# Kernel tuning notes

Measured on AMD Instinct MI355X. Metric: run time of the kernel, lower is better.

The kernel has to match this reference:

```python
import jax, jax.numpy as jnp
import numpy as np

N, E, G = 100000, 1600000, 1024
BN_EPS = 1e-5
NEG_SLOPE = 0.2


def setup_inputs() -> dict:
    key = jax.random.key(0)
    ks = jax.random.split(key, 8)
    x = jax.random.normal(ks[0], (N, 128), dtype=jnp.float32)
    edge_index = jax.random.randint(ks[1], (2, E), 0, N, dtype=jnp.int64)
    batch = jnp.sort(jax.random.randint(ks[2], (N,), 0, G, dtype=jnp.int64))
    Wl = jax.random.normal(ks[3], (3, 128, 128), dtype=jnp.float32) * 0.08
    bl = jnp.zeros((3, 128), dtype=jnp.float32)
    Wr = jax.random.normal(ks[4], (3, 128, 128), dtype=jnp.float32) * 0.08
    bn_gamma = jnp.ones((3, 128), dtype=jnp.float32)
    bn_beta = jnp.zeros((3, 128), dtype=jnp.float32)
    bn2_gamma = jnp.ones((128,), dtype=jnp.float32)
    bn2_beta = jnp.zeros((128,), dtype=jnp.float32)
    fc_W = jax.random.normal(ks[5], (128, 64), dtype=jnp.float32) * 0.08
    fc_b = jnp.zeros((64,), dtype=jnp.float32)
    return {"x": x, "edge_index": edge_index, "batch": batch, "Wl": Wl, "bl": bl,
            "Wr": Wr, "bn_gamma": bn_gamma, "bn_beta": bn_beta,
            "bn2_gamma": bn2_gamma, "bn2_beta": bn2_beta, "fc_W": fc_W, "fc_b": fc_b}


def _batch_norm(h, gamma, beta):
    # training-mode BatchNorm1d: batch statistics, biased variance
    mu = jnp.mean(h, axis=0)
    var = jnp.mean((h - mu) ** 2, axis=0)
    return gamma * (h - mu) * jax.lax.rsqrt(var + BN_EPS) + beta


def reference(x, edge_index, batch, Wl, bl, Wr, bn_gamma, bn_beta,
              bn2_gamma, bn2_beta, fc_W, fc_b):
    src, dst = edge_index[0], edge_index[1]
    # in-degree of each destination node (for mean aggregation)
    deg = jax.ops.segment_sum(jnp.ones((E,), dtype=x.dtype), dst, num_segments=N)
    inv_deg = jnp.where(deg > 0, 1.0 / jnp.maximum(deg, 1.0), 0.0)[:, None]  # [N,1]
    h = x
    for i in range(3):
        # SAGEConv: out = lin_l(mean_{j in N(i)} h_j) + lin_r(h_i)
        agg = jax.ops.segment_sum(h[src], dst, num_segments=N) * inv_deg  # [N,H]
        h = agg @ Wl[i] + bl[i] + h @ Wr[i]
        h = jax.nn.leaky_relu(_batch_norm(h, bn_gamma[i], bn_beta[i]), NEG_SLOPE)
        # dropout omitted (eval-mode / deterministic reference)
    pooled = jax.ops.segment_sum(h, batch, num_segments=G)  # [G,H] global_add_pool
    out = _batch_norm(pooled, bn2_gamma, bn2_beta) @ fc_W + fc_b  # [G,latent]
    return out
```

## Files before the change

kernel.cpp:

```cpp
#include <hip/hip_runtime.h>

#define HD 128
#define NCOPY 32
#define BSH 8
#define BSZ 256
#define EPB 4096

typedef __attribute__((ext_vector_type(8))) short short8;
typedef __attribute__((ext_vector_type(4))) float f32x4;

union ABu { unsigned long long u[2]; short8 s8; };

__device__ inline float bf2f(ushort u) {
    union { unsigned int i; float f; } x; x.i = ((unsigned int)u) << 16; return x.f;
}
__device__ inline float bflo(unsigned int u) {
    union { unsigned int i; float f; } x; x.i = u << 16; return x.f;
}
__device__ inline float bfhi(unsigned int u) {
    union { unsigned int i; float f; } x; x.i = u & 0xffff0000u; return x.f;
}
__device__ inline ushort f2bf(float f) {
    union { float f; unsigned int i; } x; x.f = f;
    unsigned int r = x.i + 0x7FFF + ((x.i >> 16) & 1);
    return (ushort)(r >> 16);
}

__global__ __launch_bounds__(256) void k_prepcount(
        const float* __restrict__ x, ushort* __restrict__ xb, int total4,
        const float* __restrict__ Wl, const float* __restrict__ Wr,
        ushort* __restrict__ WT, int wtTotal,
        const int* __restrict__ dst, int* __restrict__ bucketCount, int E, int NB, int nPB) {
    __shared__ int hist[512];
    if (blockIdx.x < nPB) {
        for (int i = threadIdx.x; i < NB; i += 256) hist[i] = 0;
        __syncthreads();
        int e0 = blockIdx.x * EPB;
#pragma unroll
        for (int j = 0; j < 16; ++j) {
            int e = e0 + j * 256 + threadIdx.x;
            if (e < E) atomicAdd(&hist[dst[e] >> BSH], 1);
        }
        __syncthreads();
        for (int i = threadIdx.x; i < NB; i += 256)
            if (hist[i]) atomicAdd(&bucketCount[i], hist[i]);
    } else {
        int i = (blockIdx.x - nPB) * 256 + threadIdx.x;
        int stride = (gridDim.x - nPB) * 256;
        for (int idx = i; idx < total4; idx += stride) {
            float4 v = ((const float4*)x)[idx];
            ushort4 o;
            o.x = f2bf(v.x); o.y = f2bf(v.y); o.z = f2bf(v.z); o.w = f2bf(v.w);
            ((ushort4*)xb)[idx] = o;
        }
        for (int idx = i; idx < wtTotal; idx += stride) {
            int l = idx >> 15;
            int rem = idx & 32767;
            int col = rem >> 8;
            int k = rem & 255;
            float v = (k < 128) ? Wl[l * 16384 + k * 128 + col]
                                : Wr[l * 16384 + (k - 128) * 128 + col];
            WT[idx] = f2bf(v);
        }
    }
}

__global__ __launch_bounds__(256) void kp_part(const int* __restrict__ src,
                                               const int* __restrict__ dst,
                                               const int* __restrict__ bCount,
                                               int* __restrict__ gCursor,
                                               unsigned int* __restrict__ packed,
                                               int E, int NB) {
    __shared__ int bbase[512];
    __shared__ int pair[256];
    __shared__ int hist[512], lbase[512], lcur[512];
    int tid = threadIdx.x;
    int i0 = 2 * tid, i1 = 2 * tid + 1;
    int v0 = (i0 < NB) ? bCount[i0] : 0;
    int v1 = (i1 < NB) ? bCount[i1] : 0;
    pair[tid] = v0 + v1;
    __syncthreads();
    for (int off = 1; off < 256; off <<= 1) {
        int t = 0;
        if (tid >= off) t = pair[tid - off];
        __syncthreads();
        if (tid >= off) pair[tid] += t;
        __syncthreads();
    }
    int incl = pair[tid];
    bbase[i0] = incl - v0 - v1;
    bbase[i1] = incl - v1;
    for (int i = tid; i < NB; i += 256) hist[i] = 0;
    __syncthreads();

    int e0 = blockIdx.x * EPB;
    int b[16]; unsigned int w[16];
#pragma unroll
    for (int j = 0; j < 16; ++j) {
        int e = e0 + j * 256 + tid;
        b[j] = -1;
        if (e < E) {
            int d = dst[e];
            int s = src[e];
            b[j] = d >> BSH;
            w[j] = (unsigned int)s | (((unsigned int)d & (BSZ - 1)) << 17);
            atomicAdd(&hist[b[j]], 1);
        }
    }
    __syncthreads();
    for (int i = tid; i < NB; i += 256) {
        int c = hist[i];
        lbase[i] = c ? (bbase[i] + atomicAdd(&gCursor[i], c)) : 0;
        lcur[i] = 0;
    }
    __syncthreads();
#pragma unroll
    for (int j = 0; j < 16; ++j) {
        if (b[j] >= 0) {
            int r = atomicAdd(&lcur[b[j]], 1);
            packed[lbase[b[j]] + r] = w[j];
        }
    }
}

__global__ __launch_bounds__(256) void kp_degfill(const unsigned int* __restrict__ packed,
                                                  const int* __restrict__ bCount,
                                                  int* __restrict__ rowptr,
                                                  float* __restrict__ inv,
                                                  int* __restrict__ csr, int N, int E, int NB) {
    __shared__ int dcnt[BSZ];
    __shared__ int scn[BSZ];
    __shared__ int rp[BSZ];
    __shared__ int red[256];
    int bkt = blockIdx.x;
    int tid = threadIdx.x;
    int n0 = bkt << BSH;
    int partial = 0;
    for (int i = tid; i < bkt; i += 256) partial += bCount[i];
    red[tid] = partial;
    __syncthreads();
    for (int off = 128; off > 0; off >>= 1) {
        if (tid < off) red[tid] += red[tid + off];
        __syncthreads();
    }
    int beg = red[0];
    int end = beg + bCount[bkt];
    __syncthreads();
    dcnt[tid] = 0;
    __syncthreads();
    for (int e = beg + tid; e < end; e += 256)
        atomicAdd(&dcnt[packed[e] >> 17], 1);
    __syncthreads();
    int v = dcnt[tid];
    scn[tid] = v;
    __syncthreads();
    for (int off = 1; off < 256; off <<= 1) {
        int t = 0;
        if (tid >= off) t = scn[tid - off];
        __syncthreads();
        if (tid >= off) scn[tid] += t;
        __syncthreads();
    }
    int rpv = beg + scn[tid] - v;
    int n = n0 + tid;
    if (n < N) {
        rowptr[n] = rpv;
        inv[n] = (v > 0) ? (1.0f / (float)v) : 0.0f;
    }
    if (bkt == 0 && tid == 0) rowptr[N] = E;
    __syncthreads();
    dcnt[tid] = 0;
    rp[tid] = rpv;
    __syncthreads();
    for (int e = beg + tid; e < end; e += 256) {
        unsigned int wv = packed[e];
        int ld = wv >> 17;
        int p = atomicAdd(&dcnt[ld], 1);
        csr[rp[ld] + p] = (int)(wv & 0x1FFFF);
    }
}

__global__ __launch_bounds__(256) void k_agg(const ushort* __restrict__ h,
                                             const int* __restrict__ rowptr,
                                             const int* __restrict__ csr,
                                             const float* __restrict__ inv,
                                             ushort* __restrict__ agg, int N) {
    int node = blockIdx.x * 4 + (threadIdx.x >> 6);
    if (node >= N) return;
    int lane = threadIdx.x & 63;
    int g = lane >> 4, ln = lane & 15;
    int beg = rowptr[node], end = rowptr[node + 1];
    float a[8], b[8];
#pragma unroll
    for (int j = 0; j < 8; ++j) { a[j] = 0.f; b[j] = 0.f; }
    for (int e = beg + g; e < end; e += 8) {
        int s0 = csr[e];
        uint4 v0 = *(const uint4*)&h[(size_t)s0 * HD + ln * 8];
        int e1 = e + 4;
        if (e1 < end) {
            int s1 = csr[e1];
            uint4 v1 = *(const uint4*)&h[(size_t)s1 * HD + ln * 8];
            b[0] += bflo(v1.x); b[1] += bfhi(v1.x);
            b[2] += bflo(v1.y); b[3] += bfhi(v1.y);
            b[4] += bflo(v1.z); b[5] += bfhi(v1.z);
            b[6] += bflo(v1.w); b[7] += bfhi(v1.w);
        }
        a[0] += bflo(v0.x); a[1] += bfhi(v0.x);
        a[2] += bflo(v0.y); a[3] += bfhi(v0.y);
        a[4] += bflo(v0.z); a[5] += bfhi(v0.z);
        a[6] += bflo(v0.w); a[7] += bfhi(v0.w);
    }
#pragma unroll
    for (int j = 0; j < 8; ++j) {
        a[j] += b[j];
        a[j] += __shfl_xor(a[j], 16);
        a[j] += __shfl_xor(a[j], 32);
    }
    if (lane < 16) {
        float iv = inv[node];
        ushort o[8];
#pragma unroll
        for (int j = 0; j < 8; ++j) o[j] = f2bf(a[j] * iv);
        *(uint4*)&agg[(size_t)node * HD + ln * 8] = *(uint4*)o;
    }
}

__global__ __launch_bounds__(256) void k_gemm(
        const ushort* __restrict__ X1, const ushort* __restrict__ X2,
        const ushort* __restrict__ WT, const float* __restrict__ bias,
        ushort* __restrict__ out, float* __restrict__ stats, int N) {
    __shared__ ushort As[128 * 72];
    __shared__ ushort Bs[128 * 72];
    int tid = threadIdx.x;
    int lane = tid & 63, wid = tid >> 6;
    int wr = wid >> 1, wc = wid & 1;
    int ln15 = lane & 15, kg = lane >> 4;
    int rbase = blockIdx.x * 128;

    f32x4 acc[4][4];
#pragma unroll
    for (int m = 0; m < 4; ++m)
#pragma unroll
        for (int nn = 0; nn < 4; ++nn) acc[m][nn] = (f32x4){0.f, 0.f, 0.f, 0.f};

    for (int c = 0; c < 4; ++c) {
        const ushort* X = (c < 2) ? X1 : X2;
        int cb = (c & 1) * 64;
#pragma unroll
        for (int p = 0; p < 4; ++p) {
            int g = tid + p * 256;
            int r = g >> 3, q = g & 7;
            int grow = rbase + r;
            uint4 v = {0u, 0u, 0u, 0u};
            if (grow < N) v = *(const uint4*)&X[(size_t)grow * HD + cb + q * 8];
            *(uint4*)&As[r * 72 + q * 8] = v;
        }
#pragma unroll
        for (int p = 0; p < 4; ++p) {
            int g = tid + p * 256;
            int col = g >> 3, q = g & 7;
            *(uint4*)&Bs[col * 72 + q * 8] = *(const uint4*)&WT[col * 256 + c * 64 + q * 8];
        }
        __syncthreads();
#pragma unroll
        for (int kk = 0; kk < 2; ++kk) {
            short8 af[4], bfr[4];
#pragma unroll
            for (int m = 0; m < 4; ++m) {
                int row = wr * 64 + m * 16 + ln15;
                const ushort* pa = &As[row * 72 + kk * 32 + kg * 4];
                ABu u; u.u[0] = *(const unsigned long long*)pa;
                u.u[1] = *(const unsigned long long*)(pa + 16);
                af[m] = u.s8;
            }
#pragma unroll
            for (int nn = 0; nn < 4; ++nn) {
                int col = wc * 64 + nn * 16 + ln15;
                const ushort* pb = &Bs[col * 72 + kk * 32 + kg * 4];
                ABu u; u.u[0] = *(const unsigned long long*)pb;
                u.u[1] = *(const unsigned long long*)(pb + 16);
                bfr[nn] = u.s8;
            }
#pragma unroll
            for (int m = 0; m < 4; ++m)
#pragma unroll
                for (int nn = 0; nn < 4; ++nn)
                    acc[m][nn] = __builtin_amdgcn_mfma_f32_16x16x32_bf16(af[m], bfr[nn], acc[m][nn], 0, 0, 0);
        }
        __syncthreads();
    }

    float s[4] = {0.f, 0.f, 0.f, 0.f};
    float q[4] = {0.f, 0.f, 0.f, 0.f};
    float bv[4];
#pragma unroll
    for (int nn = 0; nn < 4; ++nn) bv[nn] = bias[wc * 64 + nn * 16 + ln15];
#pragma unroll
    for (int m = 0; m < 4; ++m) {
#pragma unroll
        for (int j = 0; j < 4; ++j) {
            int row = rbase + wr * 64 + m * 16 + kg * 4 + j;
            if (row < N) {
#pragma unroll
                for (int nn = 0; nn < 4; ++nn) {
                    float v = acc[m][nn][j] + bv[nn];
                    out[(size_t)row * HD + wc * 64 + nn * 16 + ln15] = f2bf(v);
                    s[nn] += v; q[nn] += v * v;
                }
            }
        }
    }
#pragma unroll
    for (int nn = 0; nn < 4; ++nn) {
        s[nn] += __shfl_xor(s[nn], 16); s[nn] += __shfl_xor(s[nn], 32);
        q[nn] += __shfl_xor(q[nn], 16); q[nn] += __shfl_xor(q[nn], 32);
    }
    if (lane < 16) {
        int slot = (blockIdx.x & (NCOPY - 1)) * 256;
#pragma unroll
        for (int nn = 0; nn < 4; ++nn) {
            int col = wc * 64 + nn * 16 + lane;
            atomicAdd(&stats[slot + col], s[nn]);
            atomicAdd(&stats[slot + 128 + col], q[nn]);
        }
    }
}

__global__ __launch_bounds__(256) void k_apply(ushort* buf, const float* __restrict__ stats,
                                               const float* __restrict__ gamma,
                                               const float* __restrict__ beta,
                                               float count, int total8) {
    __shared__ float sc[HD], sh[HD];
    int tid = threadIdx.x;
    if (tid < HD) {
        float s = 0.f, q = 0.f;
        for (int i = 0; i < NCOPY; ++i) { s += stats[i * 256 + tid]; q += stats[i * 256 + 128 + tid]; }
        float mean = s / count;
        float var = fmaxf(q / count - mean * mean, 0.f);
        float scale = gamma[tid] * rsqrtf(var + 1e-5f);
        sc[tid] = scale;
        sh[tid] = beta[tid] - mean * scale;
    }
    __syncthreads();
    int i = blockIdx.x * blockDim.x + tid;
    int stride = gridDim.x * blockDim.x;
    for (int idx = i; idx < total8; idx += stride) {
        int cb = (idx * 8) & (HD - 1);
        uint4 v = ((const uint4*)buf)[idx];
        float f[8];
        f[0] = bflo(v.x); f[1] = bfhi(v.x);
        f[2] = bflo(v.y); f[3] = bfhi(v.y);
        f[4] = bflo(v.z); f[5] = bfhi(v.z);
        f[6] = bflo(v.w); f[7] = bfhi(v.w);
        ushort o[8];
#pragma unroll
        for (int j = 0; j < 8; ++j) {
            float y = f[j] * sc[cb + j] + sh[cb + j];
            y = (y > 0.f) ? y : 0.2f * y;
            o[j] = f2bf(y);
        }
        ((uint4*)buf)[idx] = *(uint4*)o;
    }
}

__global__ void k_poolapply(const ushort* __restrict__ h, const float* __restrict__ stats,
                            const float* __restrict__ gamma, const float* __restrict__ beta,
                            float count, const int* __restrict__ batch,
                            float* __restrict__ pooled, int N) {
    int c = threadIdx.x;
    float s = 0.f, q = 0.f;
    for (int i = 0; i < NCOPY; ++i) { s += stats[i * 256 + c]; q += stats[i * 256 + 128 + c]; }
    float mean = s / count;
    float var = fmaxf(q / count - mean * mean, 0.f);
    float sc = gamma[c] * rsqrtf(var + 1e-5f);
    float sh = beta[c] - mean * sc;
    int n0 = blockIdx.x * 64;
    if (n0 >= N) return;
    int nend = min(n0 + 64, N);
    float acc = 0.f;
    int cur = batch[n0];
    for (int n = n0; n < nend; ++n) {
        int b = batch[n];
        if (b != cur) { atomicAdd(&pooled[cur * HD + c], acc); acc = 0.f; cur = b; }
        float y = bf2f(h[(size_t)n * HD + c]) * sc + sh;
        y = (y > 0.f) ? y : 0.2f * y;
        acc += y;
    }
    atomicAdd(&pooled[cur * HD + c], acc);
}

__global__ void k_colstats(const float* __restrict__ X, float* __restrict__ stats, int rows) {
    int c = threadIdx.x;
    float s = 0.f, q = 0.f;
    for (int r = blockIdx.x; r < rows; r += gridDim.x) {
        float v = X[r * HD + c];
        s += v; q += v * v;
    }
    int slot = (blockIdx.x & (NCOPY - 1)) * 256;
    atomicAdd(&stats[slot + c], s);
    atomicAdd(&stats[slot + 128 + c], q);
}

__global__ void k_final(const float* __restrict__ pooled, const float* __restrict__ stats2,
                        const float* __restrict__ bn2g, const float* __restrict__ bn2b,
                        const float* __restrict__ fcW, const float* __restrict__ fcb,
                        float* __restrict__ outp, float countG) {
    __shared__ float Wlds[HD * 64];
    __shared__ float prow[HD];
    int tid = threadIdx.x;
    for (int i = tid; i < HD * 64 / 4; i += 128) ((float4*)Wlds)[i] = ((const float4*)fcW)[i];
    float s = 0.f, q = 0.f;
    for (int i = 0; i < NCOPY; ++i) { s += stats2[i * 256 + tid]; q += stats2[i * 256 + 128 + tid]; }
    float mean = s / countG;
    float var = fmaxf(q / countG - mean * mean, 0.f);
    float scale = bn2g[tid] * rsqrtf(var + 1e-5f);
    float shift = bn2b[tid] - mean * scale;
    int g = blockIdx.x;
    prow[tid] = pooled[g * HD + tid] * scale + shift;
    __syncthreads();
    if (tid < 64) {
        float acc = fcb[tid];
#pragma unroll 8
        for (int c = 0; c < HD; ++c) acc += prow[c] * Wlds[c * 64 + tid];
        outp[g * 64 + tid] = acc;
    }
}

extern "C" void kernel_launch(void* const* d_in, const int* in_sizes, int n_in,
                              void* d_out, int out_size, void* d_ws, size_t ws_size,
                              hipStream_t stream) {
    const float* x     = (const float*)d_in[0];
    const int*   ei    = (const int*)d_in[1];
    const int*   batch = (const int*)d_in[2];
    const float* Wl    = (const float*)d_in[3];
    const float* bl    = (const float*)d_in[4];
    const float* Wr    = (const float*)d_in[5];
    const float* bng   = (const float*)d_in[6];
    const float* bnb   = (const float*)d_in[7];
    const float* bn2g  = (const float*)d_in[8];
    const float* bn2b  = (const float*)d_in[9];
    const float* fcW   = (const float*)d_in[10];
    const float* fcb   = (const float*)d_in[11];

    int N = in_sizes[0] / HD;
    int E = in_sizes[1] / 2;
    int G = out_size / 64;
    const int* src = ei;
    const int* dst = ei + E;

    char* p = (char*)d_ws;
    auto alloc = [&](size_t bytes) -> void* {
        void* r = (void*)p;
        p += (bytes + 255) & ~(size_t)255;
        return r;
    };
    int NB = (N + BSZ - 1) >> BSH;
    int nPB = (E + EPB - 1) / EPB;

    int*    rowptr   = (int*)alloc((size_t)(N + 1) * 4);
    int*    csr      = (int*)alloc((size_t)E * 4);
    float*  inv      = (float*)alloc((size_t)N * 4);
    ushort* WT       = (ushort*)alloc((size_t)3 * 128 * 256 * 2);
    ushort* xb       = (ushort*)alloc((size_t)N * HD * 2);
    ushort* aggb     = (ushort*)alloc((size_t)N * HD * 2);
    ushort* hb1      = (ushort*)alloc((size_t)N * HD * 2);
    ushort* hb2      = (ushort*)alloc((size_t)N * HD * 2);
    char*   zbase    = (char*)alloc(0);
    float*  statsAll = (float*)alloc((size_t)4 * NCOPY * 256 * 4);
    float*  pooled   = (float*)alloc((size_t)G * HD * 4);
    int*    bCount   = (int*)alloc((size_t)NB * 4);
    int*    gCursor  = (int*)alloc((size_t)NB * 4);
    size_t  zbytes   = (size_t)((char*)p - zbase);

    float* stats0  = statsAll;
    float* stats1  = statsAll + NCOPY * 256;
    float* statsL2 = statsAll + 2 * NCOPY * 256;
    float* stats2  = statsAll + 3 * NCOPY * 256;

    unsigned int* packed = (unsigned int*)aggb;

    float* outp = (float*)d_out;
    int total4 = N * HD / 4;
    int total8 = N * HD / 8;
    int ggrid = (N + 127) / 128;
    int agrid = (N + 3) / 4;
    float fN = (float)N, fG = (float)G;

    hipMemsetAsync(zbase, 0, zbytes, stream);
    k_prepcount<<<nPB + 1024, 256, 0, stream>>>(x, xb, total4, Wl, Wr, WT, 3 * 128 * 256,
                                                dst, bCount, E, NB, nPB);
    kp_part<<<nPB, 256, 0, stream>>>(src, dst, bCount, gCursor, packed, E, NB);
    kp_degfill<<<NB, 256, 0, stream>>>(packed, bCount, rowptr, inv, csr, N, E, NB);

    k_agg<<<agrid, 256, 0, stream>>>(xb, rowptr, csr, inv, aggb, N);
    k_gemm<<<ggrid, 256, 0, stream>>>(aggb, xb, WT, bl, hb1, stats0, N);
    k_apply<<<2048, 256, 0, stream>>>(hb1, stats0, bng, bnb, fN, total8);

    k_agg<<<agrid, 256, 0, stream>>>(hb1, rowptr, csr, inv, aggb, N);
    k_gemm<<<ggrid, 256, 0, stream>>>(aggb, hb1, WT + 32768, bl + 128, hb2, stats1, N);
    k_apply<<<2048, 256, 0, stream>>>(hb2, stats1, bng + 128, bnb + 128, fN, total8);

    k_agg<<<agrid, 256, 0, stream>>>(hb2, rowptr, csr, inv, aggb, N);
    k_gemm<<<ggrid, 256, 0, stream>>>(aggb, hb2, WT + 65536, bl + 256, hb1, statsL2, N);
    k_poolapply<<<(N + 63) / 64, HD, 0, stream>>>(hb1, statsL2, bng + 256, bnb + 256, fN,
                                                  batch, pooled, N);

    k_colstats<<<64, HD, 0, stream>>>(pooled, stats2, G);
    k_final<<<G, HD, 0, stream>>>(pooled, stats2, bn2g, bn2b, fcW, fcb, outp, fG);
}
```

Baseline: 397.1 us.

## Overlap root-term GEMM with neighbor aggregation in one launch, split Wl GEMM

Splits the SAGE layer GEMM in two. The h@Wr + bias half runs in the same launch as the gather-based mean aggregation, on separate block ranges, so MFMA work overlaps the memory-bound gather. A second kernel then computes agg@Wl, adds it to the stored bf16 partial result, and accumulates the BN statistics. This costs an extra read-modify-write of the output in bf16, adding an extra rounding step, plus a smaller separate GEMM tile. Which blocks land on which CU also depends on how the hardware schedules the mixed grid.

```diff
diff --git a/kernel.cpp b/kernel.cpp
--- a/kernel.cpp
+++ b/kernel.cpp
@@ -180,54 +180,124 @@
     }
 }
 
-__global__ __launch_bounds__(256) void k_agg(const ushort* __restrict__ h,
-                                             const int* __restrict__ rowptr,
-                                             const int* __restrict__ csr,
-                                             const float* __restrict__ inv,
-                                             ushort* __restrict__ agg, int N) {
-    int node = blockIdx.x * 4 + (threadIdx.x >> 6);
-    if (node >= N) return;
-    int lane = threadIdx.x & 63;
-    int g = lane >> 4, ln = lane & 15;
-    int beg = rowptr[node], end = rowptr[node + 1];
-    float a[8], b[8];
-#pragma unroll
-    for (int j = 0; j < 8; ++j) { a[j] = 0.f; b[j] = 0.f; }
-    for (int e = beg + g; e < end; e += 8) {
-        int s0 = csr[e];
-        uint4 v0 = *(const uint4*)&h[(size_t)s0 * HD + ln * 8];
-        int e1 = e + 4;
-        if (e1 < end) {
-            int s1 = csr[e1];
-            uint4 v1 = *(const uint4*)&h[(size_t)s1 * HD + ln * 8];
-            b[0] += bflo(v1.x); b[1] += bfhi(v1.x);
-            b[2] += bflo(v1.y); b[3] += bfhi(v1.y);
-            b[4] += bflo(v1.z); b[5] += bfhi(v1.z);
-            b[6] += bflo(v1.w); b[7] += bfhi(v1.w);
-        }
-        a[0] += bflo(v0.x); a[1] += bfhi(v0.x);
-        a[2] += bflo(v0.y); a[3] += bfhi(v0.y);
-        a[4] += bflo(v0.z); a[5] += bfhi(v0.z);
-        a[6] += bflo(v0.w); a[7] += bfhi(v0.w);
-    }
-#pragma unroll
-    for (int j = 0; j < 8; ++j) {
-        a[j] += b[j];
-        a[j] += __shfl_xor(a[j], 16);
-        a[j] += __shfl_xor(a[j], 32);
-    }
-    if (lane < 16) {
-        float iv = inv[node];
-        ushort o[8];
-#pragma unroll
-        for (int j = 0; j < 8; ++j) o[j] = f2bf(a[j] * iv);
-        *(uint4*)&agg[(size_t)node * HD + ln * 8] = *(uint4*)o;
-    }
-}
-
-__global__ __launch_bounds__(256) void k_gemm(
-        const ushort* __restrict__ X1, const ushort* __restrict__ X2,
+__global__ __launch_bounds__(256) void k_aggemm(
+        const ushort* __restrict__ h, const int* __restrict__ rowptr,
+        const int* __restrict__ csr, const float* __restrict__ inv,
+        ushort* __restrict__ aggb,
         const ushort* __restrict__ WT, const float* __restrict__ bias,
+        ushort* __restrict__ out, int N, int gg2) {
+    __shared__ ushort As[64 * 40];
+    __shared__ ushort Bs[128 * 40];
+    int tid = threadIdx.x;
+    if ((int)blockIdx.x < gg2) {
+        int lane = tid & 63, wid = tid >> 6;
+        int wr = wid >> 1, wc = wid & 1;
+        int ln15 = lane & 15, kg = lane >> 4;
+        int rbase = blockIdx.x * 64;
+        f32x4 acc[2][4];
+#pragma unroll
+        for (int m = 0; m < 2; ++m)
+#pragma unroll
+            for (int nn = 0; nn < 4; ++nn) acc[m][nn] = (f32x4){0.f, 0.f, 0.f, 0.f};
+        int rA = tid >> 2, qA = (tid & 3) * 8;
+        for (int c = 0; c < 4; ++c) {
+            int cb = c * 32;
+            {
+                int grow = rbase + rA;
+                uint4 v = {0u, 0u, 0u, 0u};
+                if (grow < N) v = *(const uint4*)&h[(size_t)grow * HD + cb + qA];
+                *(uint4*)&As[rA * 40 + qA] = v;
+            }
+#pragma unroll
+            for (int p = 0; p < 2; ++p) {
+                int g = tid + p * 256;
+                int col = g >> 2, q = (g & 3) * 8;
+                *(uint4*)&Bs[col * 40 + q] = *(const uint4*)&WT[col * 256 + 128 + cb + q];
+            }
+            __syncthreads();
+            short8 af[2], bfr[4];
+#pragma unroll
+            for (int m = 0; m < 2; ++m) {
+                int row = wr * 32 + m * 16 + ln15;
+                const ushort* pa = &As[row * 40 + kg * 4];
+                ABu u; u.u[0] = *(const unsigned long long*)pa;
+                u.u[1] = *(const unsigned long long*)(pa + 16);
+                af[m] = u.s8;
+            }
+#pragma unroll
+            for (int nn = 0; nn < 4; ++nn) {
+                int col = wc * 64 + nn * 16 + ln15;
+                const ushort* pb = &Bs[col * 40 + kg * 4];
+                ABu u; u.u[0] = *(const unsigned long long*)pb;
+                u.u[1] = *(const unsigned long long*)(pb + 16);
+                bfr[nn] = u.s8;
+            }
+#pragma unroll
+            for (int m = 0; m < 2; ++m)
+#pragma unroll
+                for (int nn = 0; nn < 4; ++nn)
+                    acc[m][nn] = __builtin_amdgcn_mfma_f32_16x16x32_bf16(af[m], bfr[nn], acc[m][nn], 0, 0, 0);
+            __syncthreads();
+        }
+        float bv[4];
+#pragma unroll
+        for (int nn = 0; nn < 4; ++nn) bv[nn] = bias[wc * 64 + nn * 16 + ln15];
+#pragma unroll
+        for (int m = 0; m < 2; ++m) {
+#pragma unroll
+            for (int j = 0; j < 4; ++j) {
+                int row = rbase + wr * 32 + m * 16 + kg * 4 + j;
+                if (row < N) {
+#pragma unroll
+                    for (int nn = 0; nn < 4; ++nn)
+                        out[(size_t)row * HD + wc * 64 + nn * 16 + ln15] = f2bf(acc[m][nn][j] + bv[nn]);
+                }
+            }
+        }
+    } else {
+        int node = ((int)blockIdx.x - gg2) * 4 + (tid >> 6);
+        if (node >= N) return;
+        int lane = tid & 63;
+        int g = lane >> 4, ln = lane & 15;
+        int beg = rowptr[node], end = rowptr[node + 1];
+        float a[8], b[8];
+#pragma unroll
+        for (int j = 0; j < 8; ++j) { a[j] = 0.f; b[j] = 0.f; }
+        for (int e = beg + g; e < end; e += 8) {
+            int s0 = csr[e];
+            uint4 v0 = *(const uint4*)&h[(size_t)s0 * HD + ln * 8];
+            int e1 = e + 4;
+            if (e1 < end) {
+                int s1 = csr[e1];
+                uint4 v1 = *(const uint4*)&h[(size_t)s1 * HD + ln * 8];
+                b[0] += bflo(v1.x); b[1] += bfhi(v1.x);
+                b[2] += bflo(v1.y); b[3] += bfhi(v1.y);
+                b[4] += bflo(v1.z); b[5] += bfhi(v1.z);
+                b[6] += bflo(v1.w); b[7] += bfhi(v1.w);
+            }
+            a[0] += bflo(v0.x); a[1] += bfhi(v0.x);
+            a[2] += bflo(v0.y); a[3] += bfhi(v0.y);
+            a[4] += bflo(v0.z); a[5] += bfhi(v0.z);
+            a[6] += bflo(v0.w); a[7] += bfhi(v0.w);
+        }
+#pragma unroll
+        for (int j = 0; j < 8; ++j) {
+            a[j] += b[j];
+            a[j] += __shfl_xor(a[j], 16);
+            a[j] += __shfl_xor(a[j], 32);
+        }
+        if (lane < 16) {
+            float iv = inv[node];
+            ushort o[8];
+#pragma unroll
+            for (int j = 0; j < 8; ++j) o[j] = f2bf(a[j] * iv);
+            *(uint4*)&aggb[(size_t)node * HD + ln * 8] = *(uint4*)o;
+        }
+    }
+}
+
+__global__ __launch_bounds__(256) void k_gemmWl(
+        const ushort* __restrict__ X, const ushort* __restrict__ WT,
         ushort* __restrict__ out, float* __restrict__ stats, int N) {
     __shared__ ushort As[128 * 72];
     __shared__ ushort Bs[128 * 72];
@@ -243,9 +313,8 @@
 #pragma unroll
         for (int nn = 0; nn < 4; ++nn) acc[m][nn] = (f32x4){0.f, 0.f, 0.f, 0.f};
 
-    for (int c = 0; c < 4; ++c) {
-        const ushort* X = (c < 2) ? X1 : X2;
-        int cb = (c & 1) * 64;
+    for (int c = 0; c < 2; ++c) {
+        int cb = c * 64;
 #pragma unroll
         for (int p = 0; p < 4; ++p) {
             int g = tid + p * 256;
@@ -259,7 +328,7 @@
         for (int p = 0; p < 4; ++p) {
             int g = tid + p * 256;
             int col = g >> 3, q = g & 7;
-            *(uint4*)&Bs[col * 72 + q * 8] = *(const uint4*)&WT[col * 256 + c * 64 + q * 8];
+            *(uint4*)&Bs[col * 72 + q * 8] = *(const uint4*)&WT[col * 256 + cb + q * 8];
         }
         __syncthreads();
 #pragma unroll
@@ -292,9 +361,6 @@
 
     float s[4] = {0.f, 0.f, 0.f, 0.f};
     float q[4] = {0.f, 0.f, 0.f, 0.f};
-    float bv[4];
-#pragma unroll
-    for (int nn = 0; nn < 4; ++nn) bv[nn] = bias[wc * 64 + nn * 16 + ln15];
 #pragma unroll
     for (int m = 0; m < 4; ++m) {
 #pragma unroll
@@ -303,8 +369,9 @@
             if (row < N) {
 #pragma unroll
                 for (int nn = 0; nn < 4; ++nn) {
-                    float v = acc[m][nn][j] + bv[nn];
-                    out[(size_t)row * HD + wc * 64 + nn * 16 + ln15] = f2bf(v);
+                    size_t oidx = (size_t)row * HD + wc * 64 + nn * 16 + ln15;
+                    float v = acc[m][nn][j] + bf2f(out[oidx]);
+                    out[oidx] = f2bf(v);
                     s[nn] += v; q[nn] += v * v;
                 }
             }
@@ -482,6 +549,7 @@
     float* outp = (float*)d_out;
     int total4 = N * HD / 4;
     int total8 = N * HD / 8;
+    int gg2   = (N + 63) / 64;
     int ggrid = (N + 127) / 128;
     int agrid = (N + 3) / 4;
     float fN = (float)N, fG = (float)G;
@@ -492,16 +560,16 @@
     kp_part<<<nPB, 256, 0, stream>>>(src, dst, bCount, gCursor, packed, E, NB);
     kp_degfill<<<NB, 256, 0, stream>>>(packed, bCount, rowptr, inv, csr, N, E, NB);
 
-    k_agg<<<agrid, 256, 0, stream>>>(xb, rowptr, csr, inv, aggb, N);
-    k_gemm<<<ggrid, 256, 0, stream>>>(aggb, xb, WT, bl, hb1, stats0, N);
+    k_aggemm<<<gg2 + agrid, 256, 0, stream>>>(xb, rowptr, csr, inv, aggb, WT, bl, hb1, N, gg2);
+    k_gemmWl<<<ggrid, 256, 0, stream>>>(aggb, WT, hb1, stats0, N);
     k_apply<<<2048, 256, 0, stream>>>(hb1, stats0, bng, bnb, fN, total8);
 
-    k_agg<<<agrid, 256, 0, stream>>>(hb1, rowptr, csr, inv, aggb, N);
-    k_gemm<<<ggrid, 256, 0, stream>>>(aggb, hb1, WT + 32768, bl + 128, hb2, stats1, N);
+    k_aggemm<<<gg2 + agrid, 256, 0, stream>>>(hb1, rowptr, csr, inv, aggb, WT + 32768, bl + 128, hb2, N, gg2);
+    k_gemmWl<<<ggrid, 256, 0, stream>>>(aggb, WT + 32768, hb2, stats1, N);
     k_apply<<<2048, 256, 0, stream>>>(hb2, stats1, bng + 128, bnb + 128, fN, total8);
 
-    k_agg<<<agrid, 256, 0, stream>>>(hb2, rowptr, csr, inv, aggb, N);
-    k_gemm<<<ggrid, 256, 0, stream>>>(aggb, hb2, WT + 65536, bl + 256, hb1, statsL2, N);
+    k_aggemm<<<gg2 + agrid, 256, 0, stream>>>(hb2, rowptr, csr, inv, aggb, WT + 65536, bl + 256, hb1, N, gg2);
+    k_gemmWl<<<ggrid, 256, 0, stream>>>(aggb, WT + 65536, hb1, statsL2, N);
     k_poolapply<<<(N + 63) / 64, HD, 0, stream>>>(hb1, statsL2, bng + 256, bnb + 256, fN,
                                                   batch, pooled, N);
 
```

Measured after the change: 489.2 us. 23.2% more time.

## Load GEMM tiles directly into LDS with XOR-swizzled layout

Applied to the files above, without the earlier changes.

The GEMM now fills its A and B shared-memory tiles with global_load_lds, skipping the staging through registers. The padded 72-stride tiles are replaced by unpadded 64-wide rows with an XOR swizzle to avoid bank conflicts. The weight matrix is pre-swizzled on the device in the prep kernel so that B loads become contiguous per wave. Out-of-range rows are clamped to N-1 rather than zero-filled, and the GEMM still waits at a full barrier after each chunk, so the load latency is not overlapped.

```diff
diff --git a/kernel.cpp b/kernel.cpp
--- a/kernel.cpp
+++ b/kernel.cpp
@@ -11,6 +11,9 @@
 
 union ABu { unsigned long long u[2]; short8 s8; };
 
+typedef const __attribute__((address_space(1))) void* gas_t;
+typedef __attribute__((address_space(3))) void* las_t;
+
 __device__ inline float bf2f(ushort u) {
     union { unsigned int i; float f; } x; x.i = ((unsigned int)u) << 16; return x.f;
 }
@@ -26,10 +29,23 @@
     return (ushort)(r >> 16);
 }
 
+__device__ inline short8 frag_read(const ushort* tile, int row, int kk, int kg) {
+    const char* rowp = (const char*)(tile + row * 64);
+    int sw = (row & 7) << 4;
+    int b0 = kk * 64 + kg * 8;
+    int a0 = (b0 & 15) | ((b0 & ~15) ^ sw);
+    int b1 = b0 + 32;
+    int a1 = (b1 & 15) | ((b1 & ~15) ^ sw);
+    ABu u;
+    u.u[0] = *(const unsigned long long*)(rowp + a0);
+    u.u[1] = *(const unsigned long long*)(rowp + a1);
+    return u.s8;
+}
+
 __global__ __launch_bounds__(256) void k_prepcount(
         const float* __restrict__ x, ushort* __restrict__ xb, int total4,
         const float* __restrict__ Wl, const float* __restrict__ Wr,
-        ushort* __restrict__ WT, int wtTotal,
+        ushort* __restrict__ WTS, int wtTotal,
         const int* __restrict__ dst, int* __restrict__ bucketCount, int E, int NB, int nPB) {
     __shared__ int hist[512];
     if (blockIdx.x < nPB) {
@@ -55,12 +71,17 @@
         }
         for (int idx = i; idx < wtTotal; idx += stride) {
             int l = idx >> 15;
-            int rem = idx & 32767;
-            int col = rem >> 8;
-            int k = rem & 255;
+            int r = idx & 32767;
+            int c = r >> 13;
+            int r2 = r & 8191;
+            int col = r2 >> 6;
+            int kin = r2 & 63;
+            int sb = kin >> 3, j = kin & 7;
+            int b = sb ^ (col & 7);
+            int k = c * 64 + b * 8 + j;
             float v = (k < 128) ? Wl[l * 16384 + k * 128 + col]
                                 : Wr[l * 16384 + (k - 128) * 128 + col];
-            WT[idx] = f2bf(v);
+            WTS[idx] = f2bf(v);
         }
     }
 }
@@ -227,15 +248,17 @@
 
 __global__ __launch_bounds__(256) void k_gemm(
         const ushort* __restrict__ X1, const ushort* __restrict__ X2,
-        const ushort* __restrict__ WT, const float* __restrict__ bias,
+        const ushort* __restrict__ WTS, const float* __restrict__ bias,
         ushort* __restrict__ out, float* __restrict__ stats, int N) {
-    __shared__ ushort As[128 * 72];
-    __shared__ ushort Bs[128 * 72];
+    __shared__ ushort As[128 * 64];
+    __shared__ ushort Bs[128 * 64];
     int tid = threadIdx.x;
     int lane = tid & 63, wid = tid >> 6;
     int wr = wid >> 1, wc = wid & 1;
     int ln15 = lane & 15, kg = lane >> 4;
     int rbase = blockIdx.x * 128;
+    int lrow = lane >> 3;
+    int sb = lane & 7;
 
     f32x4 acc[4][4];
 #pragma unroll
@@ -245,42 +268,32 @@
 
     for (int c = 0; c < 4; ++c) {
         const ushort* X = (c < 2) ? X1 : X2;
-        int cb = (c & 1) * 64;
+        size_t cbyte = (size_t)(c & 1) * 128;
+        const char* bsrc = (const char*)WTS + (size_t)c * 16384;
 #pragma unroll
         for (int p = 0; p < 4; ++p) {
-            int g = tid + p * 256;
-            int r = g >> 3, q = g & 7;
-            int grow = rbase + r;
-            uint4 v = {0u, 0u, 0u, 0u};
-            if (grow < N) v = *(const uint4*)&X[(size_t)grow * HD + cb + q * 8];
-            *(uint4*)&As[r * 72 + q * 8] = v;
-        }
-#pragma unroll
-        for (int p = 0; p < 4; ++p) {
-            int g = tid + p * 256;
-            int col = g >> 3, q = g & 7;
-            *(uint4*)&Bs[col * 72 + q * 8] = *(const uint4*)&WT[col * 256 + c * 64 + q * 8];
+            int instr = wid * 4 + p;
+            int row_local = instr * 8 + lrow;
+            int grow = rbase + row_local;
+            if (grow >= N) grow = N - 1;
+            const char* gpA = (const char*)X + (size_t)grow * 256 + cbyte
+                              + (((sb ^ (row_local & 7)) << 4));
+            __builtin_amdgcn_global_load_lds((gas_t)gpA,
+                    (las_t)((char*)As + instr * 1024), 16, 0, 0);
+            const char* gpB = bsrc + instr * 1024 + lane * 16;
+            __builtin_amdgcn_global_load_lds((gas_t)gpB,
+                    (las_t)((char*)Bs + instr * 1024), 16, 0, 0);
         }
         __syncthreads();
 #pragma unroll
         for (int kk = 0; kk < 2; ++kk) {
             short8 af[4], bfr[4];
 #pragma unroll
-            for (int m = 0; m < 4; ++m) {
-                int row = wr * 64 + m * 16 + ln15;
-                const ushort* pa = &As[row * 72 + kk * 32 + kg * 4];
-                ABu u; u.u[0] = *(const unsigned long long*)pa;
-                u.u[1] = *(const unsigned long long*)(pa + 16);
-                af[m] = u.s8;
-            }
-#pragma unroll
-            for (int nn = 0; nn < 4; ++nn) {
-                int col = wc * 64 + nn * 16 + ln15;
-                const ushort* pb = &Bs[col * 72 + kk * 32 + kg * 4];
-                ABu u; u.u[0] = *(const unsigned long long*)pb;
-                u.u[1] = *(const unsigned long long*)(pb + 16);
-                bfr[nn] = u.s8;
-            }
+            for (int m = 0; m < 4; ++m)
+                af[m] = frag_read(As, wr * 64 + m * 16 + ln15, kk, kg);
+#pragma unroll
+            for (int nn = 0; nn < 4; ++nn)
+                bfr[nn] = frag_read(Bs, wc * 64 + nn * 16 + ln15, kk, kg);
 #pragma unroll
             for (int m = 0; m < 4; ++m)
 #pragma unroll
@@ -460,7 +473,7 @@
     int*    rowptr   = (int*)alloc((size_t)(N + 1) * 4);
     int*    csr      = (int*)alloc((size_t)E * 4);
     float*  inv      = (float*)alloc((size_t)N * 4);
-    ushort* WT       = (ushort*)alloc((size_t)3 * 128 * 256 * 2);
+    ushort* WTS      = (ushort*)alloc((size_t)3 * 128 * 256 * 2);
     ushort* xb       = (ushort*)alloc((size_t)N * HD * 2);
     ushort* aggb     = (ushort*)alloc((size_t)N * HD * 2);
     ushort* hb1      = (ushort*)alloc((size_t)N * HD * 2);
@@ -487,21 +500,21 @@
     float fN = (float)N, fG = (float)G;
 
     hipMemsetAsync(zbase, 0, zbytes, stream);
-    k_prepcount<<<nPB + 1024, 256, 0, stream>>>(x, xb, total4, Wl, Wr, WT, 3 * 128 * 256,
+    k_prepcount<<<nPB + 1024, 256, 0, stream>>>(x, xb, total4, Wl, Wr, WTS, 3 * 128 * 256,
                                                 dst, bCount, E, NB, nPB);
     kp_part<<<nPB, 256, 0, stream>>>(src, dst, bCount, gCursor, packed, E, NB);
     kp_degfill<<<NB, 256, 0, stream>>>(packed, bCount, rowptr, inv, csr, N, E, NB);
 
     k_agg<<<agrid, 256, 0, stream>>>(xb, rowptr, csr, inv, aggb, N);
-    k_gemm<<<ggrid, 256, 0, stream>>>(aggb, xb, WT, bl, hb1, stats0, N);
+    k_gemm<<<ggrid, 256, 0, stream>>>(aggb, xb, WTS, bl, hb1, stats0, N);
     k_apply<<<2048, 256, 0, stream>>>(hb1, stats0, bng, bnb, fN, total8);
 
     k_agg<<<agrid, 256, 0, stream>>>(hb1, rowptr, csr, inv, aggb, N);
-    k_gemm<<<ggrid, 256, 0, stream>>>(aggb, hb1, WT + 32768, bl + 128, hb2, stats1, N);
+    k_gemm<<<ggrid, 256, 0, stream>>>(aggb, hb1, WTS + 32768, bl + 128, hb2, stats1, N);
     k_apply<<<2048, 256, 0, stream>>>(hb2, stats1, bng + 128, bnb + 128, fN, total8);
 
     k_agg<<<agrid, 256, 0, stream>>>(hb2, rowptr, csr, inv, aggb, N);
-    k_gemm<<<ggrid, 256, 0, stream>>>(aggb, hb2, WT + 65536, bl + 256, hb1, statsL2, N);
+    k_gemm<<<ggrid, 256, 0, stream>>>(aggb, hb2, WTS + 65536, bl + 256, hb1, statsL2, N);
     k_poolapply<<<(N + 63) / 64, HD, 0, stream>>>(hb1, statsL2, bng + 256, bnb + 256, fN,
                                                   batch, pooled, N);
 
```

Result: faster. 381.5 us (-3.9%).
